# Optimization experiments

Hardware: AMD Instinct MI355X
Metric: run time of the kernel (lower is better)

The kernel has to match this reference:

```python
import jax, jax.numpy as jnp
import numpy as np

B, L, D, U = 4, 1024, 256, 32

def setup_inputs() -> dict:
    key = jax.random.key(0)
    k1, k2, k3, k4 = jax.random.split(key, 4)
    return {
        "inputs": jax.random.normal(k1, (B, L, D), dtype=jnp.float32),
        "Wt": jax.random.normal(k2, (D, U), dtype=jnp.float32) * (1.0 / np.sqrt(D)),
        "Wx": jax.random.normal(k3, (D, U), dtype=jnp.float32) * (1.0 / np.sqrt(D)),
        "bh": jnp.zeros((U,), dtype=jnp.float32),
        "Wa": jax.random.normal(k4, (U, 1), dtype=jnp.float32) * (1.0 / np.sqrt(U)),
        "ba": jnp.zeros((1,), dtype=jnp.float32),
    }


def reference(inputs, Wt, Wx, bh, Wa, ba):
    # inputs: [B, L, D]
    q = jnp.einsum('bld,du->blu', inputs, Wt)  # [B, L, U]
    k = jnp.einsum('bld,du->blu', inputs, Wx)  # [B, L, U]
    # additive (Bahdanau) pairwise score: h is [B, L, L, U]
    h = jnp.tanh(q[:, :, None, :] + k[:, None, :, :] + bh)
    e = jnp.einsum('biju,u->bij', h, Wa[:, 0]) + ba[0]  # [B, L, L]
    a = jax.nn.softmax(e, axis=-1)  # stable softmax == exp(e-max)/sum
    v = jnp.einsum('bij,bjd->bid', a, inputs)  # weighted sum, [B, L, D]
    return v
```

## Files before the change

kernel.cpp:

```cpp
#include <hip/hip_runtime.h>
#include <hip/hip_bf16.h>
#include <math.h>

#define B_ 4
#define L_ 1024
#define D_ 256
#define U_ 32
#define KSPLIT 4

#define SC2 2.8853900817779268f

#if __has_builtin(__builtin_amdgcn_exp2f)
#define EXP2(x) __builtin_amdgcn_exp2f(x)
#else
#define EXP2(x) exp2f(x)
#endif
#if __has_builtin(__builtin_amdgcn_rcpf)
#define RCP(x) __builtin_amdgcn_rcpf(x)
#else
#define RCP(x) (1.0f / (x))
#endif

typedef __attribute__((ext_vector_type(8))) short bf16x8;
typedef __attribute__((ext_vector_type(4))) float f32x4;
typedef unsigned long long u64;

__device__ __forceinline__ ushort f2bf(float f) {
  uint b = __float_as_uint(f);
  return (ushort)((b + 0x7fffu + ((b >> 16) & 1u)) >> 16);
}
__device__ __forceinline__ float bf2f(ushort u) {
  return __uint_as_float(((uint)u) << 16);
}
__device__ __forceinline__ uint packhl(float v) {
  ushort h = f2bf(v);
  ushort l = f2bf(v - bf2f(h));
  return (((uint)h) << 16) | (uint)l;
}
__device__ __forceinline__ u64 hi64(uint4 p) {
  return ((u64)(p.x >> 16)) | ((u64)(p.y >> 16) << 16) |
         ((u64)(p.z >> 16) << 32) | ((u64)(p.w >> 16) << 48);
}
__device__ __forceinline__ u64 lo64(uint4 p) {
  return ((u64)(p.x & 0xffffu)) | ((u64)(p.y & 0xffffu) << 16) |
         ((u64)(p.z & 0xffffu) << 32) | ((u64)(p.w & 0xffffu) << 48);
}
__device__ __forceinline__ uint4 mk128(u64 lo, u64 hi) {
  uint4 r;
  r.x = (uint)lo; r.y = (uint)(lo >> 32);
  r.z = (uint)hi; r.w = (uint)(hi >> 32);
  return r;
}

__global__ __launch_bounds__(256) void k_proj(
    const float* __restrict__ x, const float* __restrict__ Wt,
    const float* __restrict__ Wx, const float* __restrict__ bh,
    float* __restrict__ q2, float* __restrict__ k2, uint* __restrict__ xpk) {
  const int blk = blockIdx.x;
  const int b = blk >> 6;
  const int l0 = (blk & 63) * 16;
  const int t = threadIdx.x;
  __shared__ float xr[16][D_];

  const float* xbase = x + ((size_t)(b * L_ + l0)) * D_;
  {
    const int r = t >> 4;
    const int c0 = (t & 15) * 16;
    #pragma unroll
    for (int c = 0; c < 4; ++c)
      *(float4*)&xr[r][c0 + 4 * c] = *(const float4*)&xbase[(size_t)r * D_ + c0 + 4 * c];
  }
  __syncthreads();

  {
    const int rr = t >> 4;
    const int g = t & 15;
    const int sel = g >> 3;
    const int u0 = (g & 7) * 4;
    const float* W = sel ? Wx : Wt;
    float acc0 = 0.f, acc1 = 0.f, acc2 = 0.f, acc3 = 0.f;
    #pragma unroll 8
    for (int d = 0; d < D_; ++d) {
      const float4 w4 = *(const float4*)&W[d * U_ + u0];
      const float xv = xr[rr][d];
      acc0 = fmaf(xv, w4.x, acc0);
      acc1 = fmaf(xv, w4.y, acc1);
      acc2 = fmaf(xv, w4.z, acc2);
      acc3 = fmaf(xv, w4.w, acc3);
    }
    const size_t orow = ((size_t)(b * L_ + l0 + rr)) * U_ + u0;
    if (sel == 0) {
      q2[orow]     = SC2 * (acc0 + bh[u0]);
      q2[orow + 1] = SC2 * (acc1 + bh[u0 + 1]);
      q2[orow + 2] = SC2 * (acc2 + bh[u0 + 2]);
      q2[orow + 3] = SC2 * (acc3 + bh[u0 + 3]);
    } else {
      k2[orow]     = SC2 * acc0;
      k2[orow + 1] = SC2 * acc1;
      k2[orow + 2] = SC2 * acc2;
      k2[orow + 3] = SC2 * acc3;
    }
  }

  {
    const int lq = t & 3;
    #pragma unroll
    for (int s = 0; s < 4; ++s) {
      const int d = 64 * s + (t >> 2);
      uint4 v;
      v.x = packhl(xr[lq * 4 + 0][d]);
      v.y = packhl(xr[lq * 4 + 1][d]);
      v.z = packhl(xr[lq * 4 + 2][d]);
      v.w = packhl(xr[lq * 4 + 3][d]);
      *(uint4*)&xpk[((size_t)(b * D_ + d)) * L_ + l0 + lq * 4] = v;
    }
  }
}

__global__ __launch_bounds__(512) void k_scores(
    const float* __restrict__ q2, const float* __restrict__ k2,
    const float* __restrict__ Wa, uint* __restrict__ apk) {
  const int blk = blockIdx.x;
  const int b = blk >> 7;
  const int i0 = (blk & 127) * 8;
  const int t = threadIdx.x;
  __shared__ float e_lds[8][L_];

  const float* kb = k2 + (size_t)b * L_ * U_;
  float kr0[32], kr1[32];
  #pragma unroll
  for (int c = 0; c < 8; ++c) {
    const float4 v0 = *(const float4*)&kb[(size_t)t * U_ + 4 * c];
    const float4 v1 = *(const float4*)&kb[(size_t)(t + 512) * U_ + 4 * c];
    kr0[4 * c] = v0.x; kr0[4 * c + 1] = v0.y; kr0[4 * c + 2] = v0.z; kr0[4 * c + 3] = v0.w;
    kr1[4 * c] = v1.x; kr1[4 * c + 1] = v1.y; kr1[4 * c + 2] = v1.z; kr1[4 * c + 3] = v1.w;
  }

  float wa[32];
  float sumwa = 0.f;
  #pragma unroll
  for (int u = 0; u < 32; ++u) { wa[u] = Wa[u]; sumwa += wa[u]; }

  const float* qb = q2 + ((size_t)(b * L_ + i0)) * U_;
  #pragma unroll
  for (int i = 0; i < 8; ++i) {
    float qv[32];
    #pragma unroll
    for (int u = 0; u < 32; ++u) qv[u] = qb[i * U_ + u];
    float a00 = 0.f, a01 = 0.f, a10 = 0.f, a11 = 0.f;
    #pragma unroll
    for (int u = 0; u < 32; u += 2) {
      {
        const float y0 = qv[u] + kr0[u];
        const float r0 = RCP(EXP2(y0) + 1.f);
        a00 = fmaf(wa[u], r0, a00);
        const float y1 = qv[u] + kr1[u];
        const float r1 = RCP(EXP2(y1) + 1.f);
        a10 = fmaf(wa[u], r1, a10);
      }
      {
        const float y0 = qv[u + 1] + kr0[u + 1];
        const float r0 = RCP(EXP2(y0) + 1.f);
        a01 = fmaf(wa[u + 1], r0, a01);
        const float y1 = qv[u + 1] + kr1[u + 1];
        const float r1 = RCP(EXP2(y1) + 1.f);
        a11 = fmaf(wa[u + 1], r1, a11);
      }
    }
    e_lds[i][t]       = sumwa - 2.f * (a00 + a01);
    e_lds[i][t + 512] = sumwa - 2.f * (a10 + a11);
  }
  __syncthreads();

  const int w = t >> 6;
  const int lane = t & 63;
  float ev[16];
  float m = -1e30f;
  #pragma unroll
  for (int mm = 0; mm < 16; ++mm) {
    ev[mm] = e_lds[w][lane + 64 * mm];
    m = fmaxf(m, ev[mm]);
  }
  #pragma unroll
  for (int off = 32; off >= 1; off >>= 1) m = fmaxf(m, __shfl_xor(m, off, 64));
  float s = 0.f;
  #pragma unroll
  for (int mm = 0; mm < 16; ++mm) { ev[mm] = __expf(ev[mm] - m); s += ev[mm]; }
  #pragma unroll
  for (int off = 32; off >= 1; off >>= 1) s += __shfl_xor(s, off, 64);
  const float rinv = 1.0f / s;
  uint* arow = apk + ((size_t)(b * L_ + i0 + w)) * L_;
  #pragma unroll
  for (int mm = 0; mm < 16; ++mm) arow[lane + 64 * mm] = packhl(ev[mm] * rinv);
}

#define MFMA16(A, Bf, C) __builtin_amdgcn_mfma_f32_16x16x32_bf16(A, Bf, C, 0, 0, 0)

__global__ __launch_bounds__(256) void k_wsum(
    const uint* __restrict__ apk, const uint* __restrict__ xpk,
    float* __restrict__ psum) {
  const int d0 = blockIdx.x * 64;
  const int i0 = blockIdx.y * 64;
  const int bz = blockIdx.z;
  const int b  = bz & 3;
  const int ks0 = (bz >> 2) * 256;
  const int t  = threadIdx.x;
  const int lane = t & 63;
  const int w  = t >> 6;
  const int wr = w >> 1;
  const int wc = w & 1;

  __shared__ f32x4 ldsv[4 * 64 * 8];
  char* const base = (char*)ldsv;

  const int r  = t >> 2;
  const int kq = t & 3;
  const uint* asrc = apk + ((size_t)(b * L_ + i0 + r)) * L_ + ks0 + kq * 16;
  const uint* xsrc = xpk + ((size_t)(b * D_ + d0 + r)) * L_ + ks0 + kq * 16;

  f32x4 acc00 = {0.f, 0.f, 0.f, 0.f}, acc01 = {0.f, 0.f, 0.f, 0.f};
  f32x4 acc10 = {0.f, 0.f, 0.f, 0.f}, acc11 = {0.f, 0.f, 0.f, 0.f};

  uint4 ra[4], rx[4];
  #pragma unroll
  for (int c = 0; c < 4; ++c) {
    ra[c] = *(const uint4*)(asrc + 4 * c);
    rx[c] = *(const uint4*)(xsrc + 4 * c);
  }

  for (int step = 0; step < 4; ++step) {
    __syncthreads();
    #pragma unroll
    for (int h = 0; h < 2; ++h) {
      const int ub = (kq * 2 + h) ^ (r & 7);
      const int off = r * 128 + (ub << 4);
      *(uint4*)(base + off)         = mk128(hi64(ra[2 * h]), hi64(ra[2 * h + 1]));
      *(uint4*)(base + off + 8192)  = mk128(lo64(ra[2 * h]), lo64(ra[2 * h + 1]));
      *(uint4*)(base + off + 16384) = mk128(hi64(rx[2 * h]), hi64(rx[2 * h + 1]));
      *(uint4*)(base + off + 24576) = mk128(lo64(rx[2 * h]), lo64(rx[2 * h + 1]));
    }
    if (step < 3) {
      #pragma unroll
      for (int c = 0; c < 4; ++c) {
        ra[c] = *(const uint4*)(asrc + (step + 1) * 64 + 4 * c);
        rx[c] = *(const uint4*)(xsrc + (step + 1) * 64 + 4 * c);
      }
    }
    __syncthreads();

    #pragma unroll
    for (int ks = 0; ks < 2; ++ks) {
      const int ub = ks * 4 + (lane >> 4);
      auto frag = [&](int plane, int rbase) -> bf16x8 {
        const int rr = rbase + (lane & 15);
        const int off = plane * 8192 + rr * 128 + (((ub ^ (rr & 7))) << 4);
        return *(const bf16x8*)(base + off);
      };
      const bf16x8 ah0 = frag(0, wr * 32), ah1 = frag(0, wr * 32 + 16);
      const bf16x8 al0 = frag(1, wr * 32), al1 = frag(1, wr * 32 + 16);
      const bf16x8 xh0 = frag(2, wc * 32), xh1 = frag(2, wc * 32 + 16);
      const bf16x8 xl0 = frag(3, wc * 32), xl1 = frag(3, wc * 32 + 16);
      acc00 = MFMA16(ah0, xh0, acc00); acc00 = MFMA16(al0, xh0, acc00); acc00 = MFMA16(ah0, xl0, acc00);
      acc01 = MFMA16(ah0, xh1, acc01); acc01 = MFMA16(al0, xh1, acc01); acc01 = MFMA16(ah0, xl1, acc01);
      acc10 = MFMA16(ah1, xh0, acc10); acc10 = MFMA16(al1, xh0, acc10); acc10 = MFMA16(ah1, xl0, acc10);
      acc11 = MFMA16(ah1, xh1, acc11); acc11 = MFMA16(al1, xh1, acc11); acc11 = MFMA16(ah1, xl1, acc11);
    }
  }

  const int crow = (lane >> 4) * 4;
  const int ccol = lane & 15;
  float* pb = psum + (size_t)bz * L_ * D_;
  #pragma unroll
  for (int m2 = 0; m2 < 2; ++m2) {
    #pragma unroll
    for (int n2 = 0; n2 < 2; ++n2) {
      const f32x4 acc = m2 == 0 ? (n2 == 0 ? acc00 : acc01)
                                : (n2 == 0 ? acc10 : acc11);
      const int col = d0 + wc * 32 + n2 * 16 + ccol;
      #pragma unroll
      for (int jj = 0; jj < 4; ++jj) {
        const int rowi = i0 + wr * 32 + m2 * 16 + crow + jj;
        pb[(size_t)rowi * D_ + col] = acc[jj];
      }
    }
  }
}

__global__ __launch_bounds__(256) void k_reduce(
    const float4* __restrict__ p, float4* __restrict__ o) {
  const size_t n = (size_t)B_ * L_ * D_ / 4;
  size_t i = (size_t)blockIdx.x * 256 + threadIdx.x;
  const size_t stride = (size_t)gridDim.x * 256;
  for (; i < n; i += stride) {
    const float4 a = p[i];
    const float4 b2 = p[i + n];
    const float4 c = p[i + 2 * n];
    const float4 d = p[i + 3 * n];
    float4 r;
    r.x = (a.x + b2.x) + (c.x + d.x);
    r.y = (a.y + b2.y) + (c.y + d.y);
    r.z = (a.z + b2.z) + (c.z + d.z);
    r.w = (a.w + b2.w) + (c.w + d.w);
    o[i] = r;
  }
}

extern "C" void kernel_launch(void* const* d_in, const int* in_sizes, int n_in,
                              void* d_out, int out_size, void* d_ws, size_t ws_size,
                              hipStream_t stream) {
  const float* x  = (const float*)d_in[0];
  const float* Wt = (const float*)d_in[1];
  const float* Wx = (const float*)d_in[2];
  const float* bh = (const float*)d_in[3];
  const float* Wa = (const float*)d_in[4];
  float* out = (float*)d_out;
  float* ws = (float*)d_ws;
  float* q2 = ws;
  float* k2 = ws + (size_t)B_ * L_ * U_;
  uint* apk = (uint*)(ws + (size_t)2 * B_ * L_ * U_);
  uint* xpk = apk + (size_t)B_ * L_ * L_;
  float* psum = (float*)(xpk + (size_t)B_ * D_ * L_);
  if (ws_size < (size_t)38797312) return;

  k_proj<<<B_ * L_ / 16, 256, 0, stream>>>(x, Wt, Wx, bh, q2, k2, xpk);
  k_scores<<<B_ * (L_ / 8), 512, 0, stream>>>(q2, k2, Wa, apk);
  dim3 g3(D_ / 64, L_ / 64, B_ * KSPLIT);
  k_wsum<<<g3, 256, 0, stream>>>(apk, xpk, psum);
  k_reduce<<<1024, 256, 0, stream>>>((const float4*)psum, (float4*)out);
}
```

Baseline: 134.1 us.

## Replace split-K partial-sum reduction with float atomics and retile score kernel

The separate partial-sum buffer and reduce kernel are removed. The output is now zeroed first, and each split-K block adds its tile into it with float atomic adds, which avoids writing and re-reading four full partial copies of the output. Separately, the score kernel moves to 256-thread blocks of 4 query rows, with each thread holding 4 key rows. That doubles the block count and changes register usage. Atomics make the summation order nondeterministic and add contention at the output addresses.

```diff
diff --git a/kernel.cpp b/kernel.cpp
--- a/kernel.cpp
+++ b/kernel.cpp
@@ -50,6 +50,17 @@
   r.x = (uint)lo; r.y = (uint)(lo >> 32);
   r.z = (uint)hi; r.w = (uint)(hi >> 32);
   return r;
+}
+__device__ __forceinline__ void atomAddF(float* p, float v) {
+#if defined(__HIP_PLATFORM_AMD__)
+  unsafeAtomicAdd(p, v);
+#else
+  atomicAdd(p, v);
+#endif
+}
+
+__global__ __launch_bounds__(256) void k_zero(float4* __restrict__ o) {
+  o[(size_t)blockIdx.x * 256 + threadIdx.x] = float4{0.f, 0.f, 0.f, 0.f};
 }
 
 __global__ __launch_bounds__(256) void k_proj(
@@ -117,23 +128,25 @@
   }
 }
 
-__global__ __launch_bounds__(512) void k_scores(
+__global__ __launch_bounds__(256) void k_scores(
     const float* __restrict__ q2, const float* __restrict__ k2,
     const float* __restrict__ Wa, uint* __restrict__ apk) {
   const int blk = blockIdx.x;
-  const int b = blk >> 7;
-  const int i0 = (blk & 127) * 8;
+  const int b = blk >> 8;
+  const int i0 = (blk & 255) * 4;
   const int t = threadIdx.x;
-  __shared__ float e_lds[8][L_];
+  __shared__ float e_lds[4][L_];
 
   const float* kb = k2 + (size_t)b * L_ * U_;
-  float kr0[32], kr1[32];
-  #pragma unroll
-  for (int c = 0; c < 8; ++c) {
-    const float4 v0 = *(const float4*)&kb[(size_t)t * U_ + 4 * c];
-    const float4 v1 = *(const float4*)&kb[(size_t)(t + 512) * U_ + 4 * c];
-    kr0[4 * c] = v0.x; kr0[4 * c + 1] = v0.y; kr0[4 * c + 2] = v0.z; kr0[4 * c + 3] = v0.w;
-    kr1[4 * c] = v1.x; kr1[4 * c + 1] = v1.y; kr1[4 * c + 2] = v1.z; kr1[4 * c + 3] = v1.w;
+  float kr[4][32];
+  #pragma unroll
+  for (int j = 0; j < 4; ++j) {
+    #pragma unroll
+    for (int c = 0; c < 8; ++c) {
+      const float4 v = *(const float4*)&kb[(size_t)(t + 256 * j) * U_ + 4 * c];
+      kr[j][4 * c] = v.x; kr[j][4 * c + 1] = v.y;
+      kr[j][4 * c + 2] = v.z; kr[j][4 * c + 3] = v.w;
+    }
   }
 
   float wa[32];
@@ -143,32 +156,26 @@
 
   const float* qb = q2 + ((size_t)(b * L_ + i0)) * U_;
   #pragma unroll
-  for (int i = 0; i < 8; ++i) {
+  for (int i = 0; i < 4; ++i) {
     float qv[32];
     #pragma unroll
     for (int u = 0; u < 32; ++u) qv[u] = qb[i * U_ + u];
-    float a00 = 0.f, a01 = 0.f, a10 = 0.f, a11 = 0.f;
+    float ae[4], ao[4];
+    #pragma unroll
+    for (int j = 0; j < 4; ++j) { ae[j] = 0.f; ao[j] = 0.f; }
     #pragma unroll
     for (int u = 0; u < 32; u += 2) {
-      {
-        const float y0 = qv[u] + kr0[u];
-        const float r0 = RCP(EXP2(y0) + 1.f);
-        a00 = fmaf(wa[u], r0, a00);
-        const float y1 = qv[u] + kr1[u];
-        const float r1 = RCP(EXP2(y1) + 1.f);
-        a10 = fmaf(wa[u], r1, a10);
+      #pragma unroll
+      for (int j = 0; j < 4; ++j) {
+        const float y0 = qv[u] + kr[j][u];
+        ae[j] = fmaf(wa[u], RCP(EXP2(y0) + 1.f), ae[j]);
+        const float y1 = qv[u + 1] + kr[j][u + 1];
+        ao[j] = fmaf(wa[u + 1], RCP(EXP2(y1) + 1.f), ao[j]);
       }
-      {
-        const float y0 = qv[u + 1] + kr0[u + 1];
-        const float r0 = RCP(EXP2(y0) + 1.f);
-        a01 = fmaf(wa[u + 1], r0, a01);
-        const float y1 = qv[u + 1] + kr1[u + 1];
-        const float r1 = RCP(EXP2(y1) + 1.f);
-        a11 = fmaf(wa[u + 1], r1, a11);
-      }
-    }
-    e_lds[i][t]       = sumwa - 2.f * (a00 + a01);
-    e_lds[i][t + 512] = sumwa - 2.f * (a10 + a11);
+    }
+    #pragma unroll
+    for (int j = 0; j < 4; ++j)
+      e_lds[i][t + 256 * j] = sumwa - 2.f * (ae[j] + ao[j]);
   }
   __syncthreads();
 
@@ -198,7 +205,7 @@
 
 __global__ __launch_bounds__(256) void k_wsum(
     const uint* __restrict__ apk, const uint* __restrict__ xpk,
-    float* __restrict__ psum) {
+    float* __restrict__ out) {
   const int d0 = blockIdx.x * 64;
   const int i0 = blockIdx.y * 64;
   const int bz = blockIdx.z;
@@ -269,7 +276,7 @@
 
   const int crow = (lane >> 4) * 4;
   const int ccol = lane & 15;
-  float* pb = psum + (size_t)bz * L_ * D_;
+  float* ob = out + (size_t)b * L_ * D_;
   #pragma unroll
   for (int m2 = 0; m2 < 2; ++m2) {
     #pragma unroll
@@ -280,28 +287,9 @@
       #pragma unroll
       for (int jj = 0; jj < 4; ++jj) {
         const int rowi = i0 + wr * 32 + m2 * 16 + crow + jj;
-        pb[(size_t)rowi * D_ + col] = acc[jj];
+        atomAddF(&ob[(size_t)rowi * D_ + col], acc[jj]);
       }
     }
-  }
-}
-
-__global__ __launch_bounds__(256) void k_reduce(
-    const float4* __restrict__ p, float4* __restrict__ o) {
-  const size_t n = (size_t)B_ * L_ * D_ / 4;
-  size_t i = (size_t)blockIdx.x * 256 + threadIdx.x;
-  const size_t stride = (size_t)gridDim.x * 256;
-  for (; i < n; i += stride) {
-    const float4 a = p[i];
-    const float4 b2 = p[i + n];
-    const float4 c = p[i + 2 * n];
-    const float4 d = p[i + 3 * n];
-    float4 r;
-    r.x = (a.x + b2.x) + (c.x + d.x);
-    r.y = (a.y + b2.y) + (c.y + d.y);
-    r.z = (a.z + b2.z) + (c.z + d.z);
-    r.w = (a.w + b2.w) + (c.w + d.w);
-    o[i] = r;
   }
 }
 
@@ -319,12 +307,11 @@
   float* k2 = ws + (size_t)B_ * L_ * U_;
   uint* apk = (uint*)(ws + (size_t)2 * B_ * L_ * U_);
   uint* xpk = apk + (size_t)B_ * L_ * L_;
-  float* psum = (float*)(xpk + (size_t)B_ * D_ * L_);
-  if (ws_size < (size_t)38797312) return;
-
+  if (ws_size < (size_t)22020096) return;
+
+  k_zero<<<B_ * L_ * D_ / 1024, 256, 0, stream>>>((float4*)out);
   k_proj<<<B_ * L_ / 16, 256, 0, stream>>>(x, Wt, Wx, bh, q2, k2, xpk);
-  k_scores<<<B_ * (L_ / 8), 512, 0, stream>>>(q2, k2, Wa, apk);
+  k_scores<<<B_ * (L_ / 4), 256, 0, stream>>>(q2, k2, Wa, apk);
   dim3 g3(D_ / 64, L_ / 64, B_ * KSPLIT);
-  k_wsum<<<g3, 256, 0, stream>>>(apk, xpk, psum);
-  k_reduce<<<1024, 256, 0, stream>>>((const float4*)psum, (float4*)out);
-}
+  k_wsum<<<g3, 256, 0, stream>>>(apk, xpk, out);
+}
```

New measurement: 141.1 us. 1.05x slower.
